# Performance work log

Measured on AMD Instinct MI355X. Metric: run time of the kernel, lower is better.

Reference implementation:

```python
import jax, jax.numpy as jnp
import numpy as np

E = 16          # n_routed_experts
Z = 8           # zero_expert_num
K = 4           # moe_topk
H = 1024        # hidden_size
I = 768         # moe_intermediate_size
T = 2048        # tokens
SCALE = 2.5     # routed_scaling_factor


def setup_inputs() -> dict:
    key = jax.random.key(0)
    ks = jax.random.split(key, 6)
    return {
        "hidden_states": jax.random.normal(ks[0], (T, H), dtype=jnp.float32),
        "num_global_tokens": T,
        "max_num_tokens_per_gpu": T,
        "w_router": jax.random.normal(ks[1], (E + Z, H), dtype=jnp.float32) * 0.02,
        "correction_bias": jnp.zeros((E + Z,), dtype=jnp.float32),
        "wg": jax.random.normal(ks[2], (E, I, H), dtype=jnp.float32) * 0.02,
        "wu": jax.random.normal(ks[3], (E, I, H), dtype=jnp.float32) * 0.02,
        "wd": jax.random.normal(ks[4], (E, H, I), dtype=jnp.float32) * 0.02,
    }


def reference(hidden_states, num_global_tokens, max_num_tokens_per_gpu,
              w_router, correction_bias, wg, wu, wd):
    x = hidden_states
    # ---- router gemm (always fp32) ----
    logits = x.astype(jnp.float32) @ w_router.T                      # [T, E+Z]
    # ---- DeepSeekV3-style top-k: sigmoid scores, bias only for selection ----
    scores = jax.nn.sigmoid(logits)
    _, topk_ids = jax.lax.top_k(scores + correction_bias[None, :], K)  # [T, K]
    w = jnp.take_along_axis(scores, topk_ids, axis=-1)               # [T, K]
    w = w / jnp.sum(w, axis=-1, keepdims=True)                       # renormalize
    w = w * SCALE                                                    # routed_scaling_factor
    # ---- zero-expert masking (identity type) ----
    zero_mask = topk_ids >= E                                        # [T, K]
    zero_w = jnp.sum(jnp.where(zero_mask, w, 0.0), axis=-1, keepdims=True)
    ids = jnp.where(zero_mask, 0, topk_ids)
    w = jnp.where(zero_mask, 0.0, w)
    # ---- combine weights per (token, expert); masked slots add 0.0 ----
    cw = jnp.zeros((x.shape[0], E), dtype=jnp.float32)
    cw = cw.at[jnp.arange(x.shape[0])[:, None], ids].add(w)          # [T, E]
    # ---- grouped silu-gated expert MLPs (dense compute + masked combine) ----
    g = jnp.einsum('th,eih->eti', x, wg)                             # [E, T, I]
    u = jnp.einsum('th,eih->eti', x, wu)
    a = jax.nn.silu(g) * u
    y = jnp.einsum('eti,ehi->eth', a, wd)                            # [E, T, H]
    routed = jnp.einsum('eth,te->th', y, cw)                         # [T, H]
    return routed + x * zero_w.astype(x.dtype)
```

## Files before the change

### kernel.cpp

```cpp
#include <hip/hip_runtime.h>
#include <hip/hip_bf16.h>
#include <math.h>

typedef __bf16 bf16x8 __attribute__((ext_vector_type(8)));
typedef float f32x4 __attribute__((ext_vector_type(4)));

#define T_TOK 2048
#define HD 1024
#define ID 768
#define NE 16
#define NEZ 24
#define NK 4
#define SCALE_F 2.5f

#define MFMA(a, b, c) __builtin_amdgcn_mfma_f32_16x16x32_bf16(a, b, c, 0, 0, 0)

__device__ __forceinline__ unsigned short f2bf(float f) {
  unsigned int u = __builtin_bit_cast(unsigned int, f);
  u += 0x7FFFu + ((u >> 16) & 1u);
  return (unsigned short)(u >> 16);
}

__device__ __forceinline__ bf16x8 cvt8(float4 a, float4 b) {
  bf16x8 t;
  t[0] = (__bf16)a.x; t[1] = (__bf16)a.y; t[2] = (__bf16)a.z; t[3] = (__bf16)a.w;
  t[4] = (__bf16)b.x; t[5] = (__bf16)b.y; t[6] = (__bf16)b.z; t[7] = (__bf16)b.w;
  return t;
}

__device__ __forceinline__ void gload16(const void* g, void* l) {
  __builtin_amdgcn_global_load_lds(
      (const __attribute__((address_space(1))) void*)(unsigned long long)(uintptr_t)g,
      (__attribute__((address_space(3))) void*)(uintptr_t)l, 16, 0, 0);
}

__global__ __launch_bounds__(64) void router_k(
    const float* __restrict__ x, const float* __restrict__ wr,
    const float* __restrict__ bias,
    float* __restrict__ cw, float* __restrict__ zero_w,
    unsigned short* __restrict__ xb, float* __restrict__ out) {
  const int t = blockIdx.x;
  __shared__ float xs[HD];
  __shared__ float sc[NEZ], scb[NEZ];
  __shared__ float zw_s;
  const int l = threadIdx.x;
  for (int i = l; i < HD; i += 64) {
    float v = x[(size_t)t * HD + i];
    xs[i] = v;
    xb[(size_t)t * HD + i] = f2bf(v);
  }
  __syncthreads();
  if (l < NEZ) {
    const float* w = wr + (size_t)l * HD;
    float a0 = 0.f, a1 = 0.f, a2 = 0.f, a3 = 0.f;
    for (int h = 0; h < HD; h += 4) {
      a0 = fmaf(xs[h + 0], w[h + 0], a0);
      a1 = fmaf(xs[h + 1], w[h + 1], a1);
      a2 = fmaf(xs[h + 2], w[h + 2], a2);
      a3 = fmaf(xs[h + 3], w[h + 3], a3);
    }
    float lg = (a0 + a1) + (a2 + a3);
    float s = 1.0f / (1.0f + expf(-lg));
    sc[l] = s;
    scb[l] = s + bias[l];
  }
  __syncthreads();
  if (l == 0) {
    float cwl[NE];
    for (int e = 0; e < NE; ++e) cwl[e] = 0.f;
    unsigned picked = 0;
    int ids[NK]; float wv[NK]; float ssum = 0.f;
    for (int k = 0; k < NK; ++k) {
      int best = -1; float bv = -1e30f;
      for (int e = 0; e < NEZ; ++e) {
        if ((picked >> e) & 1u) continue;
        if (scb[e] > bv) { bv = scb[e]; best = e; }
      }
      picked |= 1u << best;
      ids[k] = best; wv[k] = sc[best]; ssum += sc[best];
    }
    float zw = 0.f;
    for (int k = 0; k < NK; ++k) {
      float w = wv[k] / ssum * SCALE_F;
      if (ids[k] >= NE) zw += w; else cwl[ids[k]] += w;
    }
    for (int e = 0; e < NE; ++e) cw[(size_t)t * NE + e] = cwl[e];
    zero_w[t] = zw;
    zw_s = zw;
  }
  __syncthreads();
  const float zw = zw_s;
  for (int i = l; i < HD; i += 64) out[(size_t)t * HD + i] = xs[i] * zw;
}

__global__ void build_k(const float* __restrict__ cw, int* __restrict__ counts,
                        int* __restrict__ lists, float* __restrict__ wlist) {
  int t = blockIdx.x * blockDim.x + threadIdx.x;
  if (t >= T_TOK) return;
  for (int e = 0; e < NE; ++e) {
    float w = cw[(size_t)t * NE + e];
    if (w != 0.f) {
      int p = atomicAdd(&counts[e], 1);
      lists[e * T_TOK + p] = t;
      wlist[e * T_TOK + p] = w;
    }
  }
}

__global__ void scan_k(const int* __restrict__ counts, int* __restrict__ offs) {
  if (threadIdx.x == 0 && blockIdx.x == 0) {
    int s = 0;
    for (int e = 0; e < NE; ++e) { offs[e] = s; s += counts[e]; }
    offs[NE] = s;
  }
}

__global__ __launch_bounds__(256) void gu_k(
    const unsigned short* __restrict__ xb,
    const float* __restrict__ wg, const float* __restrict__ wu,
    const int* __restrict__ counts, const int* __restrict__ offs,
    const int* __restrict__ lists, unsigned short* __restrict__ abuf) {
  const int e = blockIdx.z;
  const int cnt = counts[e];
  const int m0 = blockIdx.y * 128;
  if (m0 >= cnt) return;
  const int n0 = blockIdx.x * 64;

  __shared__ int toks[128];
  __shared__ char lA[16384];
  __shared__ char lG[16384];
  __shared__ char lU[16384];

  const int tid = threadIdx.x;
  if (tid < 128) {
    int m = m0 + tid;
    toks[tid] = (m < cnt) ? lists[e * T_TOK + m] : 0;
  }
  __syncthreads();

  const int arow = tid >> 3;
  const int achunk = (tid & 7) ^ (arow & 7);
  const unsigned short* asrc[4];
#pragma unroll
  for (int j = 0; j < 4; ++j)
    asrc[j] = xb + (size_t)toks[j * 32 + arow] * HD + achunk * 8;
  const int brow = tid >> 4;
  const int bchunk = (tid & 15) ^ (brow & 15);
  const size_t wbase = (size_t)e * ID * HD;
  const float* gsrc[4]; const float* usrc[4];
#pragma unroll
  for (int j = 0; j < 4; ++j) {
    size_t ro = wbase + (size_t)(n0 + j * 16 + brow) * HD + bchunk * 4;
    gsrc[j] = wg + ro;
    usrc[j] = wu + ro;
  }
  char* const ldA = lA + tid * 16;
  char* const ldG = lG + tid * 16;
  char* const ldU = lU + tid * 16;

  const int wid = tid >> 6, l = tid & 63;
  const int wm = (wid >> 1) * 64, wn = (wid & 1) * 32;
  const int q = l >> 4, r = l & 15;

  f32x4 ag[4][2] = {}; f32x4 au[4][2] = {};

  for (int k0 = 0; k0 < HD; k0 += 64) {
#pragma unroll
    for (int j = 0; j < 4; ++j) {
      gload16(asrc[j] + k0, ldA + j * 4096);
      gload16(gsrc[j] + k0, ldG + j * 4096);
      gload16(usrc[j] + k0, ldU + j * 4096);
    }
    __syncthreads();
#pragma unroll
    for (int kk = 0; kk < 2; ++kk) {
      bf16x8 a[4];
#pragma unroll
      for (int fm = 0; fm < 4; ++fm) {
        int rr = wm + fm * 16 + r;
        a[fm] = *(const bf16x8*)(lA + rr * 128 + ((((kk << 2) + q) ^ (rr & 7)) << 4));
      }
#pragma unroll
      for (int fn = 0; fn < 2; ++fn) {
        int cc = wn + fn * 16 + r;
        int c0 = (kk << 3) + 2 * q;
        int sw = cc & 15;
        const char* pg = lG + cc * 256;
        const char* pu = lU + cc * 256;
        float4 g0 = *(const float4*)(pg + ((c0 ^ sw) << 4));
        float4 g1 = *(const float4*)(pg + (((c0 + 1) ^ sw) << 4));
        float4 u0 = *(const float4*)(pu + ((c0 ^ sw) << 4));
        float4 u1 = *(const float4*)(pu + (((c0 + 1) ^ sw) << 4));
        bf16x8 bg = cvt8(g0, g1), bu = cvt8(u0, u1);
#pragma unroll
        for (int fm = 0; fm < 4; ++fm) {
          ag[fm][fn] = MFMA(a[fm], bg, ag[fm][fn]);
          au[fm][fn] = MFMA(a[fm], bu, au[fm][fn]);
        }
      }
    }
    __syncthreads();
  }

  const int rowbase = offs[e] + m0;
#pragma unroll
  for (int fm = 0; fm < 4; ++fm)
#pragma unroll
    for (int fn = 0; fn < 2; ++fn)
#pragma unroll
      for (int i2 = 0; i2 < 4; ++i2) {
        int mr = wm + fm * 16 + q * 4 + i2;
        if (m0 + mr < cnt) {
          float g = ag[fm][fn][i2], u = au[fm][fn][i2];
          float s = 1.0f / (1.0f + expf(-g));
          float aa = g * s * u;
          int col = n0 + wn + fn * 16 + r;
          abuf[(size_t)(rowbase + mr) * ID + col] = f2bf(aa);
        }
      }
}

__global__ __launch_bounds__(256) void dn_k(
    const unsigned short* __restrict__ abuf,
    const float* __restrict__ wd,
    const int* __restrict__ counts, const int* __restrict__ offs,
    const int* __restrict__ lists, const float* __restrict__ wlist,
    float* __restrict__ out) {
  const int e = blockIdx.z;
  const int cnt = counts[e];
  const int m0 = blockIdx.y * 128;
  if (m0 >= cnt) return;
  const int n0 = blockIdx.x * 128;

  __shared__ int toks[128];
  __shared__ float wts[128];
  __shared__ char lA[16384];
  __shared__ char lB[32768];

  const int tid = threadIdx.x;
  if (tid < 128) {
    int m = m0 + tid;
    if (m < cnt) { toks[tid] = lists[e * T_TOK + m]; wts[tid] = wlist[e * T_TOK + m]; }
    else         { toks[tid] = 0;                    wts[tid] = 0.f; }
  }
  __syncthreads();

  const int rowbase = offs[e] + m0;
  const int arow = tid >> 3;
  const int achunk = (tid & 7) ^ (arow & 7);
  const unsigned short* asrc[4];
#pragma unroll
  for (int j = 0; j < 4; ++j) {
    int row = j * 32 + arow;
    int grow = (m0 + row < cnt) ? rowbase + row : rowbase;
    asrc[j] = abuf + (size_t)grow * ID + achunk * 8;
  }
  const int brow = tid >> 4;
  const int bchunk = (tid & 15) ^ (brow & 15);
  const float* bsrc[8];
#pragma unroll
  for (int j = 0; j < 8; ++j)
    bsrc[j] = wd + (size_t)e * HD * ID + (size_t)(n0 + j * 16 + brow) * ID + bchunk * 4;
  char* const ldA = lA + tid * 16;
  char* const ldB = lB + tid * 16;

  const int wid = tid >> 6, l = tid & 63;
  const int wm = (wid >> 1) * 64, wn = (wid & 1) * 64;
  const int q = l >> 4, r = l & 15;

  f32x4 acc[4][4] = {};

  for (int k0 = 0; k0 < ID; k0 += 64) {
#pragma unroll
    for (int j = 0; j < 4; ++j) gload16(asrc[j] + k0, ldA + j * 4096);
#pragma unroll
    for (int j = 0; j < 8; ++j) gload16(bsrc[j] + k0, ldB + j * 4096);
    __syncthreads();
#pragma unroll
    for (int kk = 0; kk < 2; ++kk) {
      bf16x8 a[4];
#pragma unroll
      for (int fm = 0; fm < 4; ++fm) {
        int rr = wm + fm * 16 + r;
        a[fm] = *(const bf16x8*)(lA + rr * 128 + ((((kk << 2) + q) ^ (rr & 7)) << 4));
      }
#pragma unroll
      for (int fn = 0; fn < 4; ++fn) {
        int cc = wn + fn * 16 + r;
        int c0 = (kk << 3) + 2 * q;
        int sw = cc & 15;
        const char* pb = lB + cc * 256;
        float4 b0 = *(const float4*)(pb + ((c0 ^ sw) << 4));
        float4 b1 = *(const float4*)(pb + (((c0 + 1) ^ sw) << 4));
        bf16x8 b = cvt8(b0, b1);
#pragma unroll
        for (int fm = 0; fm < 4; ++fm)
          acc[fm][fn] = MFMA(a[fm], b, acc[fm][fn]);
      }
    }
    __syncthreads();
  }

#pragma unroll
  for (int fm = 0; fm < 4; ++fm)
#pragma unroll
    for (int fn = 0; fn < 4; ++fn)
#pragma unroll
      for (int i2 = 0; i2 < 4; ++i2) {
        int mr = wm + fm * 16 + q * 4 + i2;
        if (m0 + mr < cnt) {
          int col = n0 + wn + fn * 16 + r;
          atomicAdd(&out[(size_t)toks[mr] * HD + col], acc[fm][fn][i2] * wts[mr]);
        }
      }
}

extern "C" void kernel_launch(void* const* d_in, const int* in_sizes, int n_in,
                              void* d_out, int out_size, void* d_ws, size_t ws_size,
                              hipStream_t stream) {
  (void)in_sizes; (void)n_in; (void)out_size; (void)ws_size;
  const float* x    = (const float*)d_in[0];
  const float* wr   = (const float*)d_in[3];
  const float* bias = (const float*)d_in[4];
  const float* wg   = (const float*)d_in[5];
  const float* wu   = (const float*)d_in[6];
  const float* wd   = (const float*)d_in[7];
  float* out = (float*)d_out;

  char* p = (char*)d_ws;
  auto alloc = [&](size_t bytes) {
    char* r = p;
    p += (bytes + 255) & ~(size_t)255;
    return r;
  };
  float* cw      = (float*)alloc((size_t)T_TOK * NE * 4);
  float* zero_w  = (float*)alloc((size_t)T_TOK * 4);
  int*   counts  = (int*)alloc(NE * 4);
  int*   offs    = (int*)alloc((NE + 1) * 4);
  int*   lists   = (int*)alloc((size_t)NE * T_TOK * 4);
  float* wlist   = (float*)alloc((size_t)NE * T_TOK * 4);
  unsigned short* xb   = (unsigned short*)alloc((size_t)T_TOK * HD * 2);
  unsigned short* abuf = (unsigned short*)alloc((size_t)(T_TOK * NK + 128) * ID * 2);
  (void)zero_w;

  hipMemsetAsync(counts, 0, NE * 4, stream);
  router_k<<<T_TOK, 64, 0, stream>>>(x, wr, bias, cw, zero_w, xb, out);
  build_k<<<T_TOK / 256, 256, 0, stream>>>(cw, counts, lists, wlist);
  scan_k<<<1, 64, 0, stream>>>(counts, offs);
  gu_k<<<dim3(ID / 64, T_TOK / 128, NE), 256, 0, stream>>>(xb, wg, wu, counts, offs, lists, abuf);
  dn_k<<<dim3(HD / 128, T_TOK / 128, NE), 256, 0, stream>>>(abuf, wd, counts, offs, lists, wlist, out);
}
```

Before: 154.6 us.

## Fuse routing list build into router and double-buffer expert GEMM LDS stages

```diff
diff --git a/kernel.cpp b/kernel.cpp
--- a/kernel.cpp
+++ b/kernel.cpp
@@ -34,76 +34,97 @@
       (__attribute__((address_space(3))) void*)(uintptr_t)l, 16, 0, 0);
 }
 
-__global__ __launch_bounds__(64) void router_k(
+__global__ __launch_bounds__(256) void router_k(
     const float* __restrict__ x, const float* __restrict__ wr,
     const float* __restrict__ bias,
-    float* __restrict__ cw, float* __restrict__ zero_w,
+    int* __restrict__ counts, int* __restrict__ lists, float* __restrict__ wlist,
     unsigned short* __restrict__ xb, float* __restrict__ out) {
-  const int t = blockIdx.x;
-  __shared__ float xs[HD];
-  __shared__ float sc[NEZ], scb[NEZ];
-  __shared__ float zw_s;
-  const int l = threadIdx.x;
-  for (int i = l; i < HD; i += 64) {
-    float v = x[(size_t)t * HD + i];
-    xs[i] = v;
-    xb[(size_t)t * HD + i] = f2bf(v);
-  }
-  __syncthreads();
-  if (l < NEZ) {
-    const float* w = wr + (size_t)l * HD;
-    float a0 = 0.f, a1 = 0.f, a2 = 0.f, a3 = 0.f;
-    for (int h = 0; h < HD; h += 4) {
-      a0 = fmaf(xs[h + 0], w[h + 0], a0);
-      a1 = fmaf(xs[h + 1], w[h + 1], a1);
-      a2 = fmaf(xs[h + 2], w[h + 2], a2);
-      a3 = fmaf(xs[h + 3], w[h + 3], a3);
-    }
-    float lg = (a0 + a1) + (a2 + a3);
-    float s = 1.0f / (1.0f + expf(-lg));
-    sc[l] = s;
-    scb[l] = s + bias[l];
-  }
-  __syncthreads();
-  if (l == 0) {
-    float cwl[NE];
-    for (int e = 0; e < NE; ++e) cwl[e] = 0.f;
-    unsigned picked = 0;
-    int ids[NK]; float wv[NK]; float ssum = 0.f;
+  const int wv = threadIdx.x >> 6, l = threadIdx.x & 63;
+  const int t0 = (blockIdx.x * 4 + wv) * 2;
+  __shared__ float s_sc[4][2][NEZ];
+  __shared__ float s_scb[4][2][NEZ];
+
+  float4 x0[4], x1[4];
+#pragma unroll
+  for (int c = 0; c < 4; ++c) {
+    x0[c] = *(const float4*)(x + (size_t)t0 * HD + c * 256 + l * 4);
+    x1[c] = *(const float4*)(x + (size_t)(t0 + 1) * HD + c * 256 + l * 4);
+  }
+#pragma unroll
+  for (int c = 0; c < 4; ++c) {
+    ushort4 h0, h1;
+    h0.x = f2bf(x0[c].x); h0.y = f2bf(x0[c].y); h0.z = f2bf(x0[c].z); h0.w = f2bf(x0[c].w);
+    h1.x = f2bf(x1[c].x); h1.y = f2bf(x1[c].y); h1.z = f2bf(x1[c].z); h1.w = f2bf(x1[c].w);
+    *(ushort4*)(xb + (size_t)t0 * HD + c * 256 + l * 4) = h0;
+    *(ushort4*)(xb + (size_t)(t0 + 1) * HD + c * 256 + l * 4) = h1;
+  }
+#pragma unroll
+  for (int e = 0; e < NEZ; ++e) {
+    float4 a0 = {0.f, 0.f, 0.f, 0.f}, a1 = {0.f, 0.f, 0.f, 0.f};
+#pragma unroll
+    for (int c = 0; c < 4; ++c) {
+      float4 w4 = *(const float4*)(wr + (size_t)e * HD + c * 256 + l * 4);
+      a0.x = fmaf(w4.x, x0[c].x, a0.x); a0.y = fmaf(w4.y, x0[c].y, a0.y);
+      a0.z = fmaf(w4.z, x0[c].z, a0.z); a0.w = fmaf(w4.w, x0[c].w, a0.w);
+      a1.x = fmaf(w4.x, x1[c].x, a1.x); a1.y = fmaf(w4.y, x1[c].y, a1.y);
+      a1.z = fmaf(w4.z, x1[c].z, a1.z); a1.w = fmaf(w4.w, x1[c].w, a1.w);
+    }
+    float r0 = (a0.x + a0.y) + (a0.z + a0.w);
+    float r1 = (a1.x + a1.y) + (a1.z + a1.w);
+#pragma unroll
+    for (int s = 1; s < 64; s <<= 1) {
+      r0 += __shfl_xor(r0, s);
+      r1 += __shfl_xor(r1, s);
+    }
+    if (l == 0) {
+      float be = bias[e];
+      float s0 = 1.f / (1.f + expf(-r0)), s1 = 1.f / (1.f + expf(-r1));
+      s_sc[wv][0][e] = s0; s_scb[wv][0][e] = s0 + be;
+      s_sc[wv][1][e] = s1; s_scb[wv][1][e] = s1 + be;
+    }
+  }
+  float zw[2];
+#pragma unroll
+  for (int tk = 0; tk < 2; ++tk) {
+    const float* sc = s_sc[wv][tk];
+    const float* scb = s_scb[wv][tk];
+    unsigned picked = 0; int ids[NK]; float wvv[NK]; float ssum = 0.f;
+#pragma unroll
     for (int k = 0; k < NK; ++k) {
-      int best = -1; float bv = -1e30f;
+      int best = 0; float bv = -1e30f;
       for (int e = 0; e < NEZ; ++e) {
-        if ((picked >> e) & 1u) continue;
-        if (scb[e] > bv) { bv = scb[e]; best = e; }
+        float v = scb[e];
+        bool take = (((picked >> e) & 1u) == 0) && (v > bv);
+        best = take ? e : best; bv = take ? v : bv;
       }
       picked |= 1u << best;
-      ids[k] = best; wv[k] = sc[best]; ssum += sc[best];
-    }
-    float zw = 0.f;
+      ids[k] = best; wvv[k] = sc[best]; ssum += sc[best];
+    }
+    float zz = 0.f;
+    const float inv = SCALE_F / ssum;
+    const int t = t0 + tk;
+#pragma unroll
     for (int k = 0; k < NK; ++k) {
-      float w = wv[k] / ssum * SCALE_F;
-      if (ids[k] >= NE) zw += w; else cwl[ids[k]] += w;
-    }
-    for (int e = 0; e < NE; ++e) cw[(size_t)t * NE + e] = cwl[e];
-    zero_w[t] = zw;
-    zw_s = zw;
-  }
-  __syncthreads();
-  const float zw = zw_s;
-  for (int i = l; i < HD; i += 64) out[(size_t)t * HD + i] = xs[i] * zw;
-}
-
-__global__ void build_k(const float* __restrict__ cw, int* __restrict__ counts,
-                        int* __restrict__ lists, float* __restrict__ wlist) {
-  int t = blockIdx.x * blockDim.x + threadIdx.x;
-  if (t >= T_TOK) return;
-  for (int e = 0; e < NE; ++e) {
-    float w = cw[(size_t)t * NE + e];
-    if (w != 0.f) {
-      int p = atomicAdd(&counts[e], 1);
-      lists[e * T_TOK + p] = t;
-      wlist[e * T_TOK + p] = w;
-    }
+      float w = wvv[k] * inv;
+      if (ids[k] >= NE) {
+        zz += w;
+      } else if (l == 0) {
+        int p = atomicAdd(&counts[ids[k]], 1);
+        lists[ids[k] * T_TOK + p] = t;
+        wlist[ids[k] * T_TOK + p] = w;
+      }
+    }
+    zw[tk] = zz;
+  }
+#pragma unroll
+  for (int c = 0; c < 4; ++c) {
+    float4 o0, o1;
+    o0.x = x0[c].x * zw[0]; o0.y = x0[c].y * zw[0];
+    o0.z = x0[c].z * zw[0]; o0.w = x0[c].w * zw[0];
+    o1.x = x1[c].x * zw[1]; o1.y = x1[c].y * zw[1];
+    o1.z = x1[c].z * zw[1]; o1.w = x1[c].w * zw[1];
+    *(float4*)(out + (size_t)t0 * HD + c * 256 + l * 4) = o0;
+    *(float4*)(out + (size_t)(t0 + 1) * HD + c * 256 + l * 4) = o1;
   }
 }
 
@@ -115,7 +136,7 @@
   }
 }
 
-__global__ __launch_bounds__(256) void gu_k(
+__global__ __launch_bounds__(256, 3) void gu_k(
     const unsigned short* __restrict__ xb,
     const float* __restrict__ wg, const float* __restrict__ wu,
     const int* __restrict__ counts, const int* __restrict__ offs,
@@ -127,9 +148,7 @@
   const int n0 = blockIdx.x * 64;
 
   __shared__ int toks[128];
-  __shared__ char lA[16384];
-  __shared__ char lG[16384];
-  __shared__ char lU[16384];
+  __shared__ char lds[2][24576];
 
   const int tid = threadIdx.x;
   if (tid < 128) {
@@ -138,25 +157,22 @@
   }
   __syncthreads();
 
-  const int arow = tid >> 3;
-  const int achunk = (tid & 7) ^ (arow & 7);
-  const unsigned short* asrc[4];
-#pragma unroll
-  for (int j = 0; j < 4; ++j)
-    asrc[j] = xb + (size_t)toks[j * 32 + arow] * HD + achunk * 8;
-  const int brow = tid >> 4;
-  const int bchunk = (tid & 15) ^ (brow & 15);
+  const unsigned short* asrc[2];
+#pragma unroll
+  for (int j = 0; j < 2; ++j) {
+    int row = j * 64 + (tid >> 2);
+    int c = ((tid & 3) - (row >> 1)) & 3;
+    asrc[j] = xb + (size_t)toks[row] * HD + c * 8;
+  }
   const size_t wbase = (size_t)e * ID * HD;
-  const float* gsrc[4]; const float* usrc[4];
-#pragma unroll
-  for (int j = 0; j < 4; ++j) {
-    size_t ro = wbase + (size_t)(n0 + j * 16 + brow) * HD + bchunk * 4;
-    gsrc[j] = wg + ro;
-    usrc[j] = wu + ro;
-  }
-  char* const ldA = lA + tid * 16;
-  char* const ldG = lG + tid * 16;
-  char* const ldU = lU + tid * 16;
+  const float* gsrc[2]; const float* usrc[2];
+#pragma unroll
+  for (int j = 0; j < 2; ++j) {
+    int row = j * 32 + (tid >> 3);
+    int c = ((tid & 7) - row) & 7;
+    size_t ro = wbase + (size_t)(n0 + row) * HD + c * 4;
+    gsrc[j] = wg + ro; usrc[j] = wu + ro;
+  }
 
   const int wid = tid >> 6, l = tid & 63;
   const int wm = (wid >> 1) * 64, wn = (wid & 1) * 32;
@@ -164,41 +180,51 @@
 
   f32x4 ag[4][2] = {}; f32x4 au[4][2] = {};
 
-  for (int k0 = 0; k0 < HD; k0 += 64) {
-#pragma unroll
-    for (int j = 0; j < 4; ++j) {
-      gload16(asrc[j] + k0, ldA + j * 4096);
-      gload16(gsrc[j] + k0, ldG + j * 4096);
-      gload16(usrc[j] + k0, ldU + j * 4096);
-    }
+  auto stage = [&](int b, int k0) {
+    char* dst = &lds[b][0] + tid * 16;
+#pragma unroll
+    for (int j = 0; j < 2; ++j) {
+      gload16(asrc[j] + k0, dst + j * 4096);
+      gload16(gsrc[j] + k0, dst + 8192 + j * 4096);
+      gload16(usrc[j] + k0, dst + 16384 + j * 4096);
+    }
+  };
+  auto comp = [&](int b) {
+    const char* base = &lds[b][0];
+    bf16x8 a[4];
+#pragma unroll
+    for (int fm = 0; fm < 4; ++fm) {
+      int rr = wm + fm * 16 + r;
+      int p = (q + (rr >> 1)) & 3;
+      a[fm] = *(const bf16x8*)(base + rr * 64 + p * 16);
+    }
+#pragma unroll
+    for (int fn = 0; fn < 2; ++fn) {
+      int cc = wn + fn * 16 + r;
+      int p0 = (2 * q + cc) & 7, p1 = (2 * q + 1 + cc) & 7;
+      const char* pg = base + 8192 + cc * 128;
+      const char* pu = base + 16384 + cc * 128;
+      float4 g0 = *(const float4*)(pg + p0 * 16);
+      float4 g1 = *(const float4*)(pg + p1 * 16);
+      float4 u0 = *(const float4*)(pu + p0 * 16);
+      float4 u1 = *(const float4*)(pu + p1 * 16);
+      bf16x8 bg = cvt8(g0, g1), bu = cvt8(u0, u1);
+#pragma unroll
+      for (int fm = 0; fm < 4; ++fm) {
+        ag[fm][fn] = MFMA(a[fm], bg, ag[fm][fn]);
+        au[fm][fn] = MFMA(a[fm], bu, au[fm][fn]);
+      }
+    }
+  };
+
+  stage(0, 0);
+  __syncthreads();
+  for (int t = 0; t < 32; t += 2) {
+    stage(1, (t + 1) * 32);
+    comp(0);
     __syncthreads();
-#pragma unroll
-    for (int kk = 0; kk < 2; ++kk) {
-      bf16x8 a[4];
-#pragma unroll
-      for (int fm = 0; fm < 4; ++fm) {
-        int rr = wm + fm * 16 + r;
-        a[fm] = *(const bf16x8*)(lA + rr * 128 + ((((kk << 2) + q) ^ (rr & 7)) << 4));
-      }
-#pragma unroll
-      for (int fn = 0; fn < 2; ++fn) {
-        int cc = wn + fn * 16 + r;
-        int c0 = (kk << 3) + 2 * q;
-        int sw = cc & 15;
-        const char* pg = lG + cc * 256;
-        const char* pu = lU + cc * 256;
-        float4 g0 = *(const float4*)(pg + ((c0 ^ sw) << 4));
-        float4 g1 = *(const float4*)(pg + (((c0 + 1) ^ sw) << 4));
-        float4 u0 = *(const float4*)(pu + ((c0 ^ sw) << 4));
-        float4 u1 = *(const float4*)(pu + (((c0 + 1) ^ sw) << 4));
-        bf16x8 bg = cvt8(g0, g1), bu = cvt8(u0, u1);
-#pragma unroll
-        for (int fm = 0; fm < 4; ++fm) {
-          ag[fm][fn] = MFMA(a[fm], bg, ag[fm][fn]);
-          au[fm][fn] = MFMA(a[fm], bu, au[fm][fn]);
-        }
-      }
-    }
+    if (t + 2 < 32) stage(0, (t + 2) * 32);
+    comp(1);
     __syncthreads();
   }
 
@@ -220,7 +246,7 @@
       }
 }
 
-__global__ __launch_bounds__(256) void dn_k(
+__global__ __launch_bounds__(256, 3) void dn_k(
     const unsigned short* __restrict__ abuf,
     const float* __restrict__ wd,
     const int* __restrict__ counts, const int* __restrict__ offs,
@@ -234,8 +260,7 @@
 
   __shared__ int toks[128];
   __shared__ float wts[128];
-  __shared__ char lA[16384];
-  __shared__ char lB[32768];
+  __shared__ char lds[2][24576];
 
   const int tid = threadIdx.x;
   if (tid < 128) {
@@ -246,23 +271,21 @@
   __syncthreads();
 
   const int rowbase = offs[e] + m0;
-  const int arow = tid >> 3;
-  const int achunk = (tid & 7) ^ (arow & 7);
-  const unsigned short* asrc[4];
+  const unsigned short* asrc[2];
+#pragma unroll
+  for (int j = 0; j < 2; ++j) {
+    int row = j * 64 + (tid >> 2);
+    int c = ((tid & 3) - (row >> 1)) & 3;
+    int grow = (m0 + row < cnt) ? rowbase + row : rowbase;
+    asrc[j] = abuf + (size_t)grow * ID + c * 8;
+  }
+  const float* bsrc[4];
 #pragma unroll
   for (int j = 0; j < 4; ++j) {
-    int row = j * 32 + arow;
-    int grow = (m0 + row < cnt) ? rowbase + row : rowbase;
-    asrc[j] = abuf + (size_t)grow * ID + achunk * 8;
-  }
-  const int brow = tid >> 4;
-  const int bchunk = (tid & 15) ^ (brow & 15);
-  const float* bsrc[8];
-#pragma unroll
-  for (int j = 0; j < 8; ++j)
-    bsrc[j] = wd + (size_t)e * HD * ID + (size_t)(n0 + j * 16 + brow) * ID + bchunk * 4;
-  char* const ldA = lA + tid * 16;
-  char* const ldB = lB + tid * 16;
+    int row = j * 32 + (tid >> 3);
+    int c = ((tid & 7) - row) & 7;
+    bsrc[j] = wd + (size_t)e * HD * ID + (size_t)(n0 + row) * ID + c * 4;
+  }
 
   const int wid = tid >> 6, l = tid & 63;
   const int wm = (wid >> 1) * 64, wn = (wid & 1) * 64;
@@ -270,34 +293,44 @@
 
   f32x4 acc[4][4] = {};
 
-  for (int k0 = 0; k0 < ID; k0 += 64) {
-#pragma unroll
-    for (int j = 0; j < 4; ++j) gload16(asrc[j] + k0, ldA + j * 4096);
-#pragma unroll
-    for (int j = 0; j < 8; ++j) gload16(bsrc[j] + k0, ldB + j * 4096);
+  auto stage = [&](int b, int k0) {
+    char* dst = &lds[b][0] + tid * 16;
+#pragma unroll
+    for (int j = 0; j < 2; ++j) gload16(asrc[j] + k0, dst + j * 4096);
+#pragma unroll
+    for (int j = 0; j < 4; ++j) gload16(bsrc[j] + k0, dst + 8192 + j * 4096);
+  };
+  auto comp = [&](int b) {
+    const char* base = &lds[b][0];
+    bf16x8 a[4];
+#pragma unroll
+    for (int fm = 0; fm < 4; ++fm) {
+      int rr = wm + fm * 16 + r;
+      int p = (q + (rr >> 1)) & 3;
+      a[fm] = *(const bf16x8*)(base + rr * 64 + p * 16);
+    }
+#pragma unroll
+    for (int fn = 0; fn < 4; ++fn) {
+      int cc = wn + fn * 16 + r;
+      int p0 = (2 * q + cc) & 7, p1 = (2 * q + 1 + cc) & 7;
+      const char* pb = base + 8192 + cc * 128;
+      float4 b0 = *(const float4*)(pb + p0 * 16);
+      float4 b1 = *(const float4*)(pb + p1 * 16);
+      bf16x8 bb = cvt8(b0, b1);
+#pragma unroll
+      for (int fm = 0; fm < 4; ++fm)
+        acc[fm][fn] = MFMA(a[fm], bb, acc[fm][fn]);
+    }
+  };
+
+  stage(0, 0);
+  __syncthreads();
+  for (int t = 0; t < 24; t += 2) {
+    stage(1, (t + 1) * 32);
+    comp(0);
     __syncthreads();
-#pragma unroll
-    for (int kk = 0; kk < 2; ++kk) {
-      bf16x8 a[4];
-#pragma unroll
-      for (int fm = 0; fm < 4; ++fm) {
-        int rr = wm + fm * 16 + r;
-        a[fm] = *(const bf16x8*)(lA + rr * 128 + ((((kk << 2) + q) ^ (rr & 7)) << 4));
-      }
-#pragma unroll
-      for (int fn = 0; fn < 4; ++fn) {
-        int cc = wn + fn * 16 + r;
-        int c0 = (kk << 3) + 2 * q;
-        int sw = cc & 15;
-        const char* pb = lB + cc * 256;
-        float4 b0 = *(const float4*)(pb + ((c0 ^ sw) << 4));
-        float4 b1 = *(const float4*)(pb + (((c0 + 1) ^ sw) << 4));
-        bf16x8 b = cvt8(b0, b1);
-#pragma unroll
-        for (int fm = 0; fm < 4; ++fm)
-          acc[fm][fn] = MFMA(a[fm], b, acc[fm][fn]);
-      }
-    }
+    if (t + 2 < 24) stage(0, (t + 2) * 32);
+    comp(1);
     __syncthreads();
   }
 
@@ -333,19 +366,15 @@
     p += (bytes + 255) & ~(size_t)255;
     return r;
   };
-  float* cw      = (float*)alloc((size_t)T_TOK * NE * 4);
-  float* zero_w  = (float*)alloc((size_t)T_TOK * 4);
   int*   counts  = (int*)alloc(NE * 4);
   int*   offs    = (int*)alloc((NE + 1) * 4);
   int*   lists   = (int*)alloc((size_t)NE * T_TOK * 4);
   float* wlist   = (float*)alloc((size_t)NE * T_TOK * 4);
   unsigned short* xb   = (unsigned short*)alloc((size_t)T_TOK * HD * 2);
   unsigned short* abuf = (unsigned short*)alloc((size_t)(T_TOK * NK + 128) * ID * 2);
-  (void)zero_w;
 
   hipMemsetAsync(counts, 0, NE * 4, stream);
-  router_k<<<T_TOK, 64, 0, stream>>>(x, wr, bias, cw, zero_w, xb, out);
-  build_k<<<T_TOK / 256, 256, 0, stream>>>(cw, counts, lists, wlist);
+  router_k<<<T_TOK / 8, 256, 0, stream>>>(x, wr, bias, counts, lists, wlist, xb, out);
   scan_k<<<1, 64, 0, stream>>>(counts, offs);
   gu_k<<<dim3(ID / 64, T_TOK / 128, NE), 256, 0, stream>>>(xb, wg, wu, counts, offs, lists, abuf);
   dn_k<<<dim3(HD / 128, T_TOK / 128, NE), 256, 0, stream>>>(abuf, wd, counts, offs, lists, wlist, out);
```

After: 211.4 us. 1.37x slower.
